# Kernel optimization log

Hardware: AMD Instinct MI355X
Metric: run time of the kernel (lower is better)

The kernel has to match this reference:

```python
import jax, jax.numpy as jnp
import numpy as np

N = 100000          # nodes
E = 3200000         # edges (avg degree 32)
F_IN = 128
HID = [128, 256, 128, 64, 32]
EPS = 1e-5


def setup_inputs() -> dict:
    key = jax.random.key(0)
    ks = jax.random.split(key, 64)
    inp = {}
    inp["x"] = jax.random.normal(ks[0], (N, F_IN), dtype=jnp.float32)
    inp["edge_index"] = jax.random.randint(ks[1], (2, E), 0, N, dtype=jnp.int64)
    dims = [F_IN] + HID
    k = 2
    for i in range(len(HID)):
        fan_in = dims[i]
        inp[f"W{i}"] = jax.random.normal(ks[k], (dims[i], dims[i + 1]), dtype=jnp.float32) / np.sqrt(fan_in); k += 1
        inp[f"b{i}"] = jnp.zeros((dims[i + 1],), dtype=jnp.float32)
        inp[f"g{i}"] = jnp.ones((dims[i + 1],), dtype=jnp.float32)
        inp[f"be{i}"] = jnp.zeros((dims[i + 1],), dtype=jnp.float32)
    inp["fc_w"] = jax.random.normal(ks[k], (HID[-1], 1), dtype=jnp.float32) / np.sqrt(HID[-1])
    inp["fc_b"] = jnp.zeros((1,), dtype=jnp.float32)
    return inp


def _gcn_forward(x, edge_index, Ws, bs, gs, bes, fc_w, fc_b):
    src, dst = edge_index[0], edge_index[1]
    # symmetric-normalized adjacency with self-loops (PyG GCNConv default,
    # edge_weight=None -> all-ones). deg = in-degree + 1 (self-loop).
    deg = jax.ops.segment_sum(jnp.ones((E,), x.dtype), dst, num_segments=N) + 1.0
    dis = jax.lax.rsqrt(deg)                 # deg^{-1/2}
    di = 1.0 / deg                           # self-loop norm deg^{-1}
    norm = (dis[src] * dis[dst])[:, None]    # [E,1]
    for W, b, g, be in zip(Ws, bs, gs, bes):
        h = x @ W                                                        # [N,d']
        x = jax.ops.segment_sum(norm * h[src], dst, num_segments=N)
        x = x + di[:, None] * h + b                                      # conv out
        mu = jnp.mean(x, axis=0)
        var = jnp.mean(jnp.square(x - mu), axis=0)
        x = (x - mu) * jax.lax.rsqrt(var + EPS) * g + be                 # BatchNorm1d
        x = jax.nn.relu(x)                                               # dropout = eval identity
    edge_emb = x[src] * x[dst]                                           # [E, 32]
    return jax.nn.sigmoid(edge_emb @ fc_w + fc_b)                        # [E, 1]


def reference(x, edge_index, W0, b0, g0, be0, W1, b1, g1, be1, W2, b2, g2, be2,
              W3, b3, g3, be3, W4, b4, g4, be4, fc_w, fc_b):
    Ws = [W0, W1, W2, W3, W4]
    bs = [b0, b1, b2, b3, b4]
    gs = [g0, g1, g2, g3, g4]
    bes = [be0, be1, be2, be3, be4]
    return _gcn_forward(x, edge_index, Ws, bs, gs, bes, fc_w, fc_b)
```

## Files before the change

kernel.cpp:

```cpp
#include <hip/hip_runtime.h>
#include <hip/hip_fp16.h>
#include <cstddef>

#define NN 100000
#define EE 3200000
#define EPSB 1e-5f
#define NB 391
#define BCAP 10240
#define BNBLK 512

typedef _Float16 half8 __attribute__((ext_vector_type(8)));
typedef float floatx4 __attribute__((ext_vector_type(4)));


__global__ __launch_bounds__(256) void k_bscat(const int* __restrict__ src,
                                               const int* __restrict__ dst,
                                               int* __restrict__ bcur,
                                               unsigned* __restrict__ barr) {
    __shared__ int hist[NB];
    __shared__ int base[NB];
    int tid = threadIdx.x;
    for (int b = tid; b < NB; b += 256) hist[b] = 0;
    __syncthreads();
    int e0 = blockIdx.x * 4096;
    int d[16], s[16];
    #pragma unroll
    for (int j = 0; j < 16; j++) {
        int e = e0 + j * 256 + tid;
        if (e < EE) {
            d[j] = dst[e];
            s[j] = src[e];
            atomicAdd(&hist[d[j] >> 8], 1);
        } else d[j] = -1;
    }
    __syncthreads();
    for (int b = tid; b < NB; b += 256) {
        int c = hist[b];
        base[b] = (c > 0) ? atomicAdd(&bcur[b], c) : 0;
        hist[b] = 0;
    }
    __syncthreads();
    #pragma unroll
    for (int j = 0; j < 16; j++) {
        if (d[j] >= 0) {
            int b = d[j] >> 8;
            int r = atomicAdd(&hist[b], 1);
            barr[(size_t)b * BCAP + base[b] + r] =
                (unsigned)s[j] | ((unsigned)(d[j] & 255) << 17);
        }
    }
}

__global__ __launch_bounds__(1024) void k_bdeg(const int* __restrict__ bcur,
                                               const unsigned* __restrict__ barr,
                                               int* __restrict__ degcnt,
                                               float* __restrict__ dis) {
    __shared__ int h[256];
    int b = blockIdx.x;
    if (threadIdx.x < 256) h[threadIdx.x] = 0;
    __syncthreads();
    int cnt = bcur[b];
    const unsigned* p = barr + (size_t)b * BCAP;
    for (int t = threadIdx.x; t < cnt; t += 1024)
        atomicAdd(&h[(p[t] >> 17) & 255], 1);
    __syncthreads();
    if (threadIdx.x < 256) {
        int node = (b << 8) + threadIdx.x;
        if (node < NN) {
            int dg = h[threadIdx.x];
            degcnt[node] = dg;
            dis[node] = rsqrtf((float)dg + 1.0f);
        }
    }
}

__global__ __launch_bounds__(1024) void k_place(const int* __restrict__ bcur,
                                                const unsigned* __restrict__ barr,
                                                const int* __restrict__ rowptr,
                                                int* __restrict__ col) {
    __shared__ int cur[256];
    int b = blockIdx.x;
    if (threadIdx.x < 256) {
        int node = (b << 8) + threadIdx.x;
        cur[threadIdx.x] = (node < NN) ? rowptr[node] : 0;
    }
    __syncthreads();
    int cnt = bcur[b];
    const unsigned* p = barr + (size_t)b * BCAP;
    for (int t = threadIdx.x; t < cnt; t += 1024) {
        unsigned e = p[t];
        int pos = atomicAdd(&cur[(e >> 17) & 255], 1);
        col[pos] = (int)(e & 0x1FFFFu);
    }
}

__global__ void k_scan_block(const int* __restrict__ in, int* __restrict__ out,
                             int* __restrict__ blksum, int n) {
    __shared__ int s[1024];
    int i = blockIdx.x * 1024 + threadIdx.x;
    int v = (i < n) ? in[i] : 0;
    s[threadIdx.x] = v;
    __syncthreads();
    for (int off = 1; off < 1024; off <<= 1) {
        int t = (threadIdx.x >= off) ? s[threadIdx.x - off] : 0;
        __syncthreads();
        s[threadIdx.x] += t;
        __syncthreads();
    }
    if (i < n) out[i] = s[threadIdx.x] - v;
    if (threadIdx.x == 1023) blksum[blockIdx.x] = s[1023];
}

__global__ void k_scan_top(int* __restrict__ blksum, int nb) {
    if (threadIdx.x == 0) {
        int acc = 0;
        for (int b = 0; b < nb; b++) { int v = blksum[b]; blksum[b] = acc; acc += v; }
    }
}

__global__ void k_scan_add(int* __restrict__ out, const int* __restrict__ blksum, int n) {
    int i = blockIdx.x * 1024 + threadIdx.x;
    if (i < n) out[i] += blksum[blockIdx.x];
}


__global__ void k_f2h(const float4* __restrict__ in, uint2* __restrict__ out, int n4) {
    int t = blockIdx.x * blockDim.x + threadIdx.x;
    if (t >= n4) return;
    float4 v = in[t];
    union { __half2 h; unsigned u; } a, b;
    a.h = __floats2half2_rn(v.x, v.y);
    b.h = __floats2half2_rn(v.z, v.w);
    out[t] = make_uint2(a.u, b.u);
}

__global__ void k_wpack_all(const float* __restrict__ W0, const float* __restrict__ W1,
                            const float* __restrict__ W2, const float* __restrict__ W3,
                            const float* __restrict__ W4, __half* __restrict__ Wp) {
    const int offs[6] = {0, 16384, 49152, 81920, 90112, 92160};
    const int Ks[5] = {128, 128, 256, 128, 64};
    const int Ns[5] = {128, 256, 128, 64, 32};
    const float* Ws[5] = {W0, W1, W2, W3, W4};
    int t = blockIdx.x * blockDim.x + threadIdx.x;
    if (t >= 92160) return;
    int l = 0;
    while (t >= offs[l + 1]) l++;
    int local = t - offs[l];
    int N = Ns[l], K = Ks[l];
    int k = local / N, n = local - k * N;
    Wp[(size_t)offs[l] + (size_t)n * K + k] = __float2half(Ws[l][local]);
}


template<int NT, bool OUT16, bool ABN>
__global__ __launch_bounds__(256) void k_mgemm(const void* __restrict__ Av,
                                               const __half* __restrict__ Wp,
                                               void* __restrict__ Cv,
                                               int M, int K, int N,
                                               const float* __restrict__ dis,
                                               const float* __restrict__ bias,
                                               const float* __restrict__ AB) {
    constexpr int TN = NT * 16;
    __shared__ __half Ash[128][40];
    __shared__ __half Bsh[TN][40];
    int tid  = threadIdx.x;
    int wave = tid >> 6;
    int lane = tid & 63;
    int quad = lane >> 4;
    int l16  = lane & 15;
    int bm = blockIdx.x * 128;
    int bn = blockIdx.y * TN;

    floatx4 acc[2][NT];
    #pragma unroll
    for (int mt = 0; mt < 2; mt++)
        #pragma unroll
        for (int nt = 0; nt < NT; nt++)
            acc[mt][nt] = (floatx4){0.f, 0.f, 0.f, 0.f};

    for (int k0 = 0; k0 < K; k0 += 32) {
        #pragma unroll
        for (int it = 0; it < 2; it++) {
            int u = tid + it * 256;
            int row = u >> 2, seg = u & 3;
            int grow = bm + row;
            if (ABN) {
                const float* Af = (const float*)Av;
                int f0 = k0 + seg * 8;
                uint4 o = make_uint4(0, 0, 0, 0);
                if (grow < M) {
                    float4 x0 = *(const float4*)&Af[(size_t)grow * K + f0];
                    float4 x1 = *(const float4*)&Af[(size_t)grow * K + f0 + 4];
                    float4 a0 = *(const float4*)&AB[f0];
                    float4 a1 = *(const float4*)&AB[f0 + 4];
                    float4 c0 = *(const float4*)&AB[K + f0];
                    float4 c1 = *(const float4*)&AB[K + f0 + 4];
                    float h0 = fmaxf(x0.x * a0.x + c0.x, 0.f);
                    float h1 = fmaxf(x0.y * a0.y + c0.y, 0.f);
                    float h2 = fmaxf(x0.z * a0.z + c0.z, 0.f);
                    float h3 = fmaxf(x0.w * a0.w + c0.w, 0.f);
                    float h4 = fmaxf(x1.x * a1.x + c1.x, 0.f);
                    float h5 = fmaxf(x1.y * a1.y + c1.y, 0.f);
                    float h6 = fmaxf(x1.z * a1.z + c1.z, 0.f);
                    float h7 = fmaxf(x1.w * a1.w + c1.w, 0.f);
                    union { __half2 h; unsigned u; } p0, p1, p2, p3;
                    p0.h = __floats2half2_rn(h0, h1);
                    p1.h = __floats2half2_rn(h2, h3);
                    p2.h = __floats2half2_rn(h4, h5);
                    p3.h = __floats2half2_rn(h6, h7);
                    o = make_uint4(p0.u, p1.u, p2.u, p3.u);
                }
                *(uint4*)&Ash[row][seg * 8] = o;
            } else {
                const __half* A = (const __half*)Av;
                uint4 v = make_uint4(0, 0, 0, 0);
                if (grow < M) v = *(const uint4*)&A[(size_t)grow * K + k0 + seg * 8];
                *(uint4*)&Ash[row][seg * 8] = v;
            }
        }
        if (tid < TN * 4) {
            int n = tid >> 2, seg = tid & 3;
            uint4 v = *(const uint4*)&Wp[(size_t)(bn + n) * K + k0 + seg * 8];
            *(uint4*)&Bsh[n][seg * 8] = v;
        }
        __syncthreads();
        half8 a[2], b[NT];
        #pragma unroll
        for (int mt = 0; mt < 2; mt++)
            a[mt] = *(const half8*)&Ash[wave * 32 + mt * 16 + l16][quad * 8];
        #pragma unroll
        for (int nt = 0; nt < NT; nt++)
            b[nt] = *(const half8*)&Bsh[nt * 16 + l16][quad * 8];
        #pragma unroll
        for (int mt = 0; mt < 2; mt++)
            #pragma unroll
            for (int nt = 0; nt < NT; nt++)
                acc[mt][nt] = __builtin_amdgcn_mfma_f32_16x16x32_f16(
                    a[mt], b[nt], acc[mt][nt], 0, 0, 0);
        __syncthreads();
    }

    #pragma unroll
    for (int mt = 0; mt < 2; mt++) {
        #pragma unroll
        for (int r = 0; r < 4; r++) {
            int grow = bm + wave * 32 + mt * 16 + quad * 4 + r;
            if (grow >= M) continue;
            if (OUT16) {
                float ds = dis[grow];
                __half* C = (__half*)Cv;
                #pragma unroll
                for (int nt = 0; nt < NT; nt++) {
                    int gcol = bn + nt * 16 + l16;
                    C[(size_t)grow * N + gcol] = __float2half(ds * acc[mt][nt][r]);
                }
            } else {
                float* C = (float*)Cv;
                #pragma unroll
                for (int nt = 0; nt < NT; nt++) {
                    int gcol = bn + nt * 16 + l16;
                    C[(size_t)grow * N + gcol] = acc[mt][nt][r] + bias[gcol];
                }
            }
        }
    }
}


__global__ __launch_bounds__(256) void k_q8p8(const uint4* __restrict__ H,
                                              uint2* __restrict__ q8,
                                              float* __restrict__ scq, int total) {
    int t = blockIdx.x * 256 + threadIdx.x;
    if (t >= total) return;
    uint4 v = H[t];
    const __half2* hp = (const __half2*)&v;
    float h[8];
    #pragma unroll
    for (int k = 0; k < 4; k++) {
        float2 f = __half22float2(hp[k]);
        h[2 * k] = f.x; h[2 * k + 1] = f.y;
    }
    float m = fabsf(h[0]);
    #pragma unroll
    for (int k = 1; k < 8; k++) m = fmaxf(m, fabsf(h[k]));
    float inv = m > 0.f ? 127.f / m : 0.f;
    unsigned b[8];
    #pragma unroll
    for (int k = 0; k < 8; k++) {
        float f = fminf(fmaxf(h[k] * inv, -127.f), 127.f);
        b[k] = (unsigned)(f + 128.5f);
    }
    q8[t] = make_uint2(b[0] | (b[1] << 8) | (b[2] << 16) | (b[3] << 24),
                       b[4] | (b[5] << 8) | (b[6] << 16) | (b[7] << 24));
    scq[t] = m * (1.f / 127.f);
}

__global__ void k_nscale_q8(const float* __restrict__ X, const float* __restrict__ AB,
                            const float* __restrict__ dis, uint2* __restrict__ q8,
                            float* __restrict__ scq) {
    int t = blockIdx.x * blockDim.x + threadIdx.x;
    if (t >= NN * 16) return;
    int row = t >> 4;
    int f0 = (t & 15) * 8;
    float ds = dis[row];
    float4 x0 = *(const float4*)&X[(size_t)row * 128 + f0];
    float4 x1 = *(const float4*)&X[(size_t)row * 128 + f0 + 4];
    float4 a0 = *(const float4*)&AB[f0];
    float4 a1 = *(const float4*)&AB[f0 + 4];
    float4 c0 = *(const float4*)&AB[128 + f0];
    float4 c1 = *(const float4*)&AB[128 + f0 + 4];
    float h[8];
    h[0] = ds * fmaxf(x0.x * a0.x + c0.x, 0.f);
    h[1] = ds * fmaxf(x0.y * a0.y + c0.y, 0.f);
    h[2] = ds * fmaxf(x0.z * a0.z + c0.z, 0.f);
    h[3] = ds * fmaxf(x0.w * a0.w + c0.w, 0.f);
    h[4] = ds * fmaxf(x1.x * a1.x + c1.x, 0.f);
    h[5] = ds * fmaxf(x1.y * a1.y + c1.y, 0.f);
    h[6] = ds * fmaxf(x1.z * a1.z + c1.z, 0.f);
    h[7] = ds * fmaxf(x1.w * a1.w + c1.w, 0.f);
    float m = h[0];
    #pragma unroll
    for (int k = 1; k < 8; k++) m = fmaxf(m, h[k]);
    m = fmaxf(m, __shfl_xor(m, 1));
    float inv = m > 0.f ? 255.f / m : 0.f;
    unsigned b[8];
    #pragma unroll
    for (int k = 0; k < 8; k++)
        b[k] = (unsigned)(fminf(h[k] * inv, 255.f) + 0.5f);
    q8[t] = make_uint2(b[0] | (b[1] << 8) | (b[2] << 16) | (b[3] << 24),
                       b[4] | (b[5] << 8) | (b[6] << 16) | (b[7] << 24));
    if ((t & 1) == 0) scq[t >> 1] = m * (1.f / 255.f);
}


__device__ __forceinline__ void acc_q8s2(float* acc, const uint4& r,
                                         const float2& s, float& c0, float& c1) {
    const unsigned* w = (const unsigned*)&r;
    c0 += s.x; c1 += s.y;
    #pragma unroll
    for (int q = 0; q < 4; q++) {
        unsigned v = w[q];
        float sq = (q < 2) ? s.x : s.y;
        acc[4 * q + 0] = fmaf(sq, (float)(v & 0xffu), acc[4 * q + 0]);
        acc[4 * q + 1] = fmaf(sq, (float)((v >> 8) & 0xffu), acc[4 * q + 1]);
        acc[4 * q + 2] = fmaf(sq, (float)((v >> 16) & 0xffu), acc[4 * q + 2]);
        acc[4 * q + 3] = fmaf(sq, (float)(v >> 24), acc[4 * q + 3]);
    }
}

template<int TPN>
__global__ __launch_bounds__(256) void k_agg_q8s(const uint4* __restrict__ Q,
                                                 const float* __restrict__ sc,
                                                 float* __restrict__ outf,
                                                 const int* __restrict__ rowptr,
                                                 const int* __restrict__ degcnt,
                                                 const int* __restrict__ colv,
                                                 const float* __restrict__ dis,
                                                 const float* __restrict__ bias) {
    constexpr int G = 256 / TPN;
    int g    = threadIdx.x / TPN;
    int lane = threadIdx.x % TPN;
    int i = blockIdx.x * G + g;
    if (i >= NN) return;
    int beg = rowptr[i];
    int cnt = degcnt[i];
    const uint4*  base = Q + lane;
    const float2* scb  = (const float2*)sc + lane;
    float acc[16] = {};
    float c0 = 0.f, c1 = 0.f;
    int e = 0;
    for (; e + 8 <= cnt; e += 8) {
        int c[8];
        #pragma unroll
        for (int j = 0; j < 8; j++) c[j] = colv[beg + e + j];
        uint4 r[8];
        float2 s[8];
        #pragma unroll
        for (int j = 0; j < 8; j++) {
            r[j] = base[(size_t)c[j] * TPN];
            s[j] = scb[(size_t)c[j] * TPN];
        }
        #pragma unroll
        for (int j = 0; j < 8; j++) acc_q8s2(acc, r[j], s[j], c0, c1);
    }
    for (; e < cnt; e++) {
        int c = colv[beg + e];
        uint4 r = base[(size_t)c * TPN];
        acc_q8s2(acc, r, scb[(size_t)c * TPN], c0, c1);
    }
    uint4 rs = base[(size_t)i * TPN];
    acc_q8s2(acc, rs, scb[(size_t)i * TPN], c0, c1);
    float ds = dis[i];
    float zp0 = 128.f * c0, zp1 = 128.f * c1;
    float o[16];
    #pragma unroll
    for (int k = 0; k < 16; k++) o[k] = ds * (acc[k] - (k < 8 ? zp0 : zp1));
    float4* out = (float4*)outf;
    const float4* bi = (const float4*)bias;
    size_t ob = (size_t)i * (4 * TPN) + lane * 4;
    #pragma unroll
    for (int j = 0; j < 4; j++) {
        float4 b = bi[lane * 4 + j];
        out[ob + j] = make_float4(o[4 * j] + b.x, o[4 * j + 1] + b.y,
                                  o[4 * j + 2] + b.z, o[4 * j + 3] + b.w);
    }
}

__device__ __forceinline__ void acc_q8u(float* acc, const uint4& r, float s) {
    const unsigned* w = (const unsigned*)&r;
    #pragma unroll
    for (int q = 0; q < 4; q++) {
        unsigned v = w[q];
        acc[4 * q + 0] = fmaf(s, (float)(v & 0xffu), acc[4 * q + 0]);
        acc[4 * q + 1] = fmaf(s, (float)((v >> 8) & 0xffu), acc[4 * q + 1]);
        acc[4 * q + 2] = fmaf(s, (float)((v >> 16) & 0xffu), acc[4 * q + 2]);
        acc[4 * q + 3] = fmaf(s, (float)(v >> 24), acc[4 * q + 3]);
    }
}

template<int TPN>
__global__ __launch_bounds__(256) void k_agg_q8u(const uint4* __restrict__ Q,
                                                 const float* __restrict__ sc,
                                                 __half* __restrict__ out16,
                                                 const int* __restrict__ rowptr,
                                                 const int* __restrict__ degcnt,
                                                 const int* __restrict__ colv,
                                                 const float* __restrict__ dis) {
    constexpr int G = 256 / TPN;
    int g    = threadIdx.x / TPN;
    int lane = threadIdx.x % TPN;
    int i = blockIdx.x * G + g;
    if (i >= NN) return;
    int beg = rowptr[i];
    int cnt = degcnt[i];
    const uint4* base = Q + lane;
    const float* scb  = sc + lane;
    float acc[16] = {};
    int e = 0;
    for (; e + 8 <= cnt; e += 8) {
        int c[8];
        #pragma unroll
        for (int j = 0; j < 8; j++) c[j] = colv[beg + e + j];
        uint4 r[8];
        float s[8];
        #pragma unroll
        for (int j = 0; j < 8; j++) {
            r[j] = base[(size_t)c[j] * TPN];
            s[j] = scb[(size_t)c[j] * TPN];
        }
        #pragma unroll
        for (int j = 0; j < 8; j++) acc_q8u(acc, r[j], s[j]);
    }
    for (; e < cnt; e++) {
        int c = colv[beg + e];
        uint4 r = base[(size_t)c * TPN];
        acc_q8u(acc, r, scb[(size_t)c * TPN]);
    }
    uint4 rs = base[(size_t)i * TPN];
    acc_q8u(acc, rs, scb[(size_t)i * TPN]);
    float ds = dis[i];
    float o[16];
    #pragma unroll
    for (int k = 0; k < 16; k++) o[k] = ds * acc[k];
    uint4 ov0, ov1;
    __half2* p0 = (__half2*)&ov0;
    __half2* p1 = (__half2*)&ov1;
    #pragma unroll
    for (int k = 0; k < 4; k++) {
        p0[k] = __floats2half2_rn(o[2 * k], o[2 * k + 1]);
        p1[k] = __floats2half2_rn(o[8 + 2 * k], o[9 + 2 * k]);
    }
    uint4* out = (uint4*)out16;
    size_t ob = (size_t)i * (2 * TPN) + lane * 2;
    out[ob]     = ov0;
    out[ob + 1] = ov1;
}

__device__ __forceinline__ void acc_row(float* acc, const uint4& r) {
    const __half2* hp = (const __half2*)&r;
    #pragma unroll
    for (int k = 0; k < 4; k++) {
        float2 f2 = __half22float2(hp[k]);
        acc[2 * k]     += f2.x;
        acc[2 * k + 1] += f2.y;
    }
}

template<int TPN, bool OUT16>
__global__ __launch_bounds__(256) void k_agg_h(const uint4* __restrict__ Hs,
                                               void* __restrict__ outv,
                                               const int* __restrict__ rowptr,
                                               const int* __restrict__ degcnt,
                                               const int* __restrict__ colv,
                                               const float* __restrict__ dis,
                                               const float* __restrict__ bias) {
    constexpr int G = 256 / TPN;
    int g    = threadIdx.x / TPN;
    int lane = threadIdx.x % TPN;
    int i = blockIdx.x * G + g;
    if (i >= NN) return;
    int beg = rowptr[i];
    int cnt = degcnt[i];
    const uint4* base = Hs + lane;
    float acc[8] = {};
    int e = 0;
    for (; e + 16 <= cnt; e += 16) {
        int c[16];
        #pragma unroll
        for (int j = 0; j < 16; j++) c[j] = colv[beg + e + j];
        uint4 r[16];
        #pragma unroll
        for (int j = 0; j < 16; j++) r[j] = base[(size_t)c[j] * TPN];
        #pragma unroll
        for (int j = 0; j < 16; j++) acc_row(acc, r[j]);
    }
    for (; e + 4 <= cnt; e += 4) {
        int c[4];
        #pragma unroll
        for (int j = 0; j < 4; j++) c[j] = colv[beg + e + j];
        uint4 r[4];
        #pragma unroll
        for (int j = 0; j < 4; j++) r[j] = base[(size_t)c[j] * TPN];
        #pragma unroll
        for (int j = 0; j < 4; j++) acc_row(acc, r[j]);
    }
    for (; e < cnt; e++) {
        uint4 r = base[(size_t)colv[beg + e] * TPN];
        acc_row(acc, r);
    }
    uint4 rs = base[(size_t)i * TPN];
    acc_row(acc, rs);
    float ds = dis[i];
    float o[8];
    #pragma unroll
    for (int k = 0; k < 8; k++) o[k] = ds * acc[k];
    if (OUT16) {
        uint4 ov;
        __half2* op = (__half2*)&ov;
        #pragma unroll
        for (int k = 0; k < 4; k++) op[k] = __floats2half2_rn(o[2 * k], o[2 * k + 1]);
        ((uint4*)outv)[(size_t)i * TPN + lane] = ov;
    } else {
        float4 b0 = ((const float4*)bias)[lane * 2];
        float4 b1 = ((const float4*)bias)[lane * 2 + 1];
        o[0] += b0.x; o[1] += b0.y; o[2] += b0.z; o[3] += b0.w;
        o[4] += b1.x; o[5] += b1.y; o[6] += b1.z; o[7] += b1.w;
        float4* out = (float4*)outv;
        size_t ob = (size_t)i * (2 * TPN) + lane * 2;
        out[ob]     = make_float4(o[0], o[1], o[2], o[3]);
        out[ob + 1] = make_float4(o[4], o[5], o[6], o[7]);
    }
}


template<int D>
__global__ __launch_bounds__(256) void k_bnpart(const float4* __restrict__ X4,
                                                float* __restrict__ partial) {
    constexpr int Q   = D / 4;
    constexpr int RPI = 256 / Q;
    int tq = threadIdx.x % Q;
    int rg = threadIdx.x / Q;
    int chunk = (NN + BNBLK - 1) / BNBLK;
    int r0 = blockIdx.x * chunk;
    int r1 = r0 + chunk; if (r1 > NN) r1 = NN;
    float4 s  = {0.f, 0.f, 0.f, 0.f};
    float4 s2 = {0.f, 0.f, 0.f, 0.f};
    for (int r = r0 + rg; r < r1; r += RPI) {
        float4 v = X4[(size_t)r * Q + tq];
        s.x += v.x; s.y += v.y; s.z += v.z; s.w += v.w;
        s2.x += v.x * v.x; s2.y += v.y * v.y; s2.z += v.z * v.z; s2.w += v.w * v.w;
    }
    __shared__ float4 ls[256], ls2[256];
    ls[threadIdx.x] = s; ls2[threadIdx.x] = s2;
    __syncthreads();
    if (threadIdx.x < Q) {
        float4 a = ls[threadIdx.x], b = ls2[threadIdx.x];
        #pragma unroll
        for (int g = 1; g < RPI; g++) {
            float4 u = ls[g * Q + threadIdx.x], w = ls2[g * Q + threadIdx.x];
            a.x += u.x; a.y += u.y; a.z += u.z; a.w += u.w;
            b.x += w.x; b.y += w.y; b.z += w.z; b.w += w.w;
        }
        *(float4*)&partial[(size_t)blockIdx.x * 2 * D + threadIdx.x * 4]     = a;
        *(float4*)&partial[(size_t)blockIdx.x * 2 * D + D + threadIdx.x * 4] = b;
    }
}

template<int D>
__global__ __launch_bounds__(1024) void k_bnfin2(const float* __restrict__ partial,
                                                 const float* __restrict__ g,
                                                 const float* __restrict__ be,
                                                 float* __restrict__ AB) {
    constexpr int G = 1024 / D;
    int f  = threadIdx.x % D;
    int gr = threadIdx.x / D;
    float sum = 0.f, sq = 0.f;
    for (int b = gr; b < BNBLK; b += G) {
        sum += partial[(size_t)b * 2 * D + f];
        sq  += partial[(size_t)b * 2 * D + D + f];
    }
    __shared__ float ls[1024], ls2[1024];
    ls[threadIdx.x] = sum; ls2[threadIdx.x] = sq;
    __syncthreads();
    if (threadIdx.x < D) {
        float a = ls[threadIdx.x], b = ls2[threadIdx.x];
        for (int k = 1; k < G; k++) {
            a += ls[k * D + threadIdx.x];
            b += ls2[k * D + threadIdx.x];
        }
        float mu  = a / (float)NN;
        float var = b / (float)NN - mu * mu;
        var = fmaxf(var, 0.f);
        float inv = rsqrtf(var + EPSB);
        float sc = g[threadIdx.x] * inv;
        AB[threadIdx.x]     = sc;
        AB[D + threadIdx.x] = be[threadIdx.x] - mu * sc;
    }
}

__global__ void k_norm16(const float4* __restrict__ X, const float* __restrict__ AB,
                         uint2* __restrict__ Y, int d, int total4) {
    int t = blockIdx.x * blockDim.x + threadIdx.x;
    if (t >= total4) return;
    int f0 = (t * 4) & (d - 1);
    float4 v = X[t];
    float a0 = AB[f0],     a1 = AB[f0 + 1], a2 = AB[f0 + 2], a3 = AB[f0 + 3];
    float c0 = AB[d + f0], c1 = AB[d + f0 + 1], c2 = AB[d + f0 + 2], c3 = AB[d + f0 + 3];
    float o0 = fmaxf(v.x * a0 + c0, 0.f);
    float o1 = fmaxf(v.y * a1 + c1, 0.f);
    float o2 = fmaxf(v.z * a2 + c2, 0.f);
    float o3 = fmaxf(v.w * a3 + c3, 0.f);
    union { __half2 h; unsigned u; } p, q;
    p.h = __floats2half2_rn(o0, o1);
    q.h = __floats2half2_rn(o2, o3);
    Y[t] = make_uint2(p.u, q.u);
}


__global__ __launch_bounds__(256) void k_edge16(const uint4* __restrict__ X,
                                                const int* __restrict__ src,
                                                const int* __restrict__ dst,
                                                const float* __restrict__ fcw,
                                                const float* __restrict__ fcb,
                                                float* __restrict__ out) {
    int lane = threadIdx.x & 3;
    size_t t = (size_t)blockIdx.x * 256 + threadIdx.x;
    int eid = (int)(t >> 2);
    if (eid >= EE) return;
    int s = src[eid], d = dst[eid];
    uint4 av = X[(size_t)s * 4 + lane];
    uint4 bv = X[(size_t)d * 4 + lane];
    const __half2* ap = (const __half2*)&av;
    const __half2* bp2 = (const __half2*)&bv;
    float v = 0.f;
    #pragma unroll
    for (int k = 0; k < 4; k++) {
        float2 fa = __half22float2(ap[k]);
        float2 fb = __half22float2(bp2[k]);
        float w0 = fcw[lane * 8 + 2 * k];
        float w1 = fcw[lane * 8 + 2 * k + 1];
        v += fa.x * fb.x * w0 + fa.y * fb.y * w1;
    }
    v += __shfl_xor(v, 1, 4);
    v += __shfl_xor(v, 2, 4);
    if (lane == 0) out[eid] = 1.f / (1.f + expf(-(v + fcb[0])));
}


extern "C" void kernel_launch(void* const* d_in, const int* in_sizes, int n_in,
                              void* d_out, int out_size, void* d_ws, size_t ws_size,
                              hipStream_t stream) {
    const float* x0 = (const float*)d_in[0];
    const int* ei   = (const int*)d_in[1];
    const int* srcv = ei;
    const int* dstv = ei + EE;
    const float *W[5], *bp[5], *gp[5], *bep[5];
    int idx = 2;
    for (int l = 0; l < 5; l++) {
        W[l]   = (const float*)d_in[idx++];
        bp[l]  = (const float*)d_in[idx++];
        gp[l]  = (const float*)d_in[idx++];
        bep[l] = (const float*)d_in[idx++];
    }
    const float* fcw = (const float*)d_in[22];
    const float* fcb = (const float*)d_in[23];

    char* ws = (char*)d_ws;
    size_t off = 0;
    auto alloc = [&](size_t bytes) -> void* {
        void* p = ws + off;
        off = (off + bytes + 255) & ~(size_t)255;
        return p;
    };
    float*    bufA    = (float*)   alloc((size_t)NN * 256 * 4);
    __half*   act16   = (__half*)  alloc((size_t)NN * 256 * 2);
    __half*   x16     = (__half*)  alloc((size_t)NN * 128 * 2);
    __half*   Hh      = (__half*)  alloc((size_t)NN * 128 * 2);
    unsigned* barr    = (unsigned*)alloc((size_t)NB * BCAP * 4);
    int*      colv    = (int*)     alloc((size_t)EE * 4);
    int*      rowptr  = (int*)     alloc((size_t)NN * 4);
    int*      degcnt  = (int*)     alloc((size_t)NN * 4);
    float*    dis     = (float*)   alloc((size_t)NN * 4);
    int*      bcur    = (int*)     alloc((size_t)NB * 4);
    int*      scnblk  = (int*)     alloc(4096);
    float*    bnpart  = (float*)   alloc((size_t)BNBLK * 512 * 4);
    float*    bnAB    = (float*)   alloc(512 * 4);
    __half*   Wp      = (__half*)  alloc((size_t)92160 * 2);
    float*    scq     = (float*)   alloc((size_t)NN * 16 * 4);
    const int woff[5] = {0, 16384, 49152, 81920, 90112};

    unsigned char* q8 = (unsigned char*)barr;

    hipMemsetAsync(bcur, 0, (size_t)NB * 4, stream);
    k_bscat<<<(EE + 4095) / 4096, 256, 0, stream>>>(srcv, dstv, bcur, barr);
    k_bdeg<<<NB, 1024, 0, stream>>>(bcur, barr, degcnt, dis);
    int nScanBlk = (NN + 1023) / 1024;
    k_scan_block<<<nScanBlk, 1024, 0, stream>>>(degcnt, rowptr, scnblk, NN);
    k_scan_top<<<1, 64, 0, stream>>>(scnblk, nScanBlk);
    k_scan_add<<<nScanBlk, 1024, 0, stream>>>(rowptr, scnblk, NN);
    k_place<<<NB, 1024, 0, stream>>>(bcur, barr, rowptr, colv);

    k_f2h<<<(NN * 128 / 4 + 255) / 256, 256, 0, stream>>>(
        (const float4*)x0, (uint2*)x16, NN * 128 / 4);
    k_wpack_all<<<(92160 + 255) / 256, 256, 0, stream>>>(W[0], W[1], W[2], W[3], W[4], Wp);

    int gx = (NN + 127) / 128;

    {
        dim3 grid(gx, 128 / 64);
        k_mgemm<4, true, false><<<grid, 256, 0, stream>>>(x16, Wp + woff[0], Hh, NN, 128, 128, dis, nullptr, nullptr);
        k_q8p8<<<NN * 16 / 256, 256, 0, stream>>>((const uint4*)Hh, (uint2*)q8, scq, NN * 16);
        k_agg_q8s<8><<<(NN + 31) / 32, 256, 0, stream>>>(
            (const uint4*)q8, scq, bufA, rowptr, degcnt, colv, dis, bp[0]);
        k_bnpart<128><<<BNBLK, 256, 0, stream>>>((const float4*)bufA, bnpart);
        k_bnfin2<128><<<1, 1024, 0, stream>>>(bnpart, gp[0], bep[0], bnAB);
        k_nscale_q8<<<(NN * 16 + 255) / 256, 256, 0, stream>>>(bufA, bnAB, dis, (uint2*)q8, scq);
    }
    {
        k_agg_q8u<8><<<(NN + 31) / 32, 256, 0, stream>>>(
            (const uint4*)q8, scq, act16, rowptr, degcnt, colv, dis);
        dim3 grid(gx, 256 / 64);
        k_mgemm<4, false, false><<<grid, 256, 0, stream>>>(act16, Wp + woff[1], bufA, NN, 128, 256, nullptr, bp[1], nullptr);
        k_bnpart<256><<<BNBLK, 256, 0, stream>>>((const float4*)bufA, bnpart);
        k_bnfin2<256><<<1, 1024, 0, stream>>>(bnpart, gp[1], bep[1], bnAB);
    }
    {
        dim3 grid(gx, 128 / 64);
        k_mgemm<4, true, true><<<grid, 256, 0, stream>>>(bufA, Wp + woff[2], Hh, NN, 256, 128, dis, nullptr, bnAB);
        k_agg_h<16, false><<<(NN + 15) / 16, 256, 0, stream>>>(
            (const uint4*)Hh, bufA, rowptr, degcnt, colv, dis, bp[2]);
        k_bnpart<128><<<BNBLK, 256, 0, stream>>>((const float4*)bufA, bnpart);
        k_bnfin2<128><<<1, 1024, 0, stream>>>(bnpart, gp[2], bep[2], bnAB);
    }
    {
        dim3 grid(gx, 64 / 64);
        k_mgemm<4, true, true><<<grid, 256, 0, stream>>>(bufA, Wp + woff[3], Hh, NN, 128, 64, dis, nullptr, bnAB);
        k_agg_h<8, false><<<(NN + 31) / 32, 256, 0, stream>>>(
            (const uint4*)Hh, bufA, rowptr, degcnt, colv, dis, bp[3]);
        k_bnpart<64><<<BNBLK, 256, 0, stream>>>((const float4*)bufA, bnpart);
        k_bnfin2<64><<<1, 1024, 0, stream>>>(bnpart, gp[3], bep[3], bnAB);
    }
    {
        dim3 grid(gx, 1);
        k_mgemm<2, true, true><<<grid, 256, 0, stream>>>(bufA, Wp + woff[4], Hh, NN, 64, 32, dis, nullptr, bnAB);
        k_agg_h<4, false><<<(NN + 63) / 64, 256, 0, stream>>>(
            (const uint4*)Hh, bufA, rowptr, degcnt, colv, dis, bp[4]);
        k_bnpart<32><<<BNBLK, 256, 0, stream>>>((const float4*)bufA, bnpart);
        k_bnfin2<32><<<1, 1024, 0, stream>>>(bnpart, gp[4], bep[4], bnAB);
        int total4 = NN * 32 / 4;
        k_norm16<<<(total4 + 255) / 256, 256, 0, stream>>>(
            (const float4*)bufA, bnAB, (uint2*)act16, 32, total4);
    }

    size_t edgeThreads = (size_t)EE * 4;
    k_edge16<<<(unsigned)((edgeThreads + 255) / 256), 256, 0, stream>>>(
        (const uint4*)act16, srcv, dstv, fcw, fcb, (float*)d_out);
}
```

Before: 984.5 us.

## Store conv outputs in fp16 and fuse BatchNorm partial sums into aggregation

Conv-layer outputs are now stored as fp16 instead of fp32. The aggregation kernels also compute per-block sum and sum-of-squares partials through shared memory. This removes most separate BatchNorm-partial passes and halves the intermediate read/write traffic. In exchange the finalize kernel reads many more partials (one per aggregation block), and storing pre-BN activations in fp16 adds precision risk.

```diff
diff --git a/kernel.cpp b/kernel.cpp
--- a/kernel.cpp
+++ b/kernel.cpp
@@ -152,7 +152,7 @@
 }
 
 
-template<int NT, bool OUT16, bool ABN>
+template<int NT, bool OUT16, bool ABN, bool AH16, bool CH16>
 __global__ __launch_bounds__(256) void k_mgemm(const void* __restrict__ Av,
                                                const __half* __restrict__ Wp,
                                                void* __restrict__ Cv,
@@ -185,24 +185,38 @@
             int row = u >> 2, seg = u & 3;
             int grow = bm + row;
             if (ABN) {
-                const float* Af = (const float*)Av;
                 int f0 = k0 + seg * 8;
                 uint4 o = make_uint4(0, 0, 0, 0);
                 if (grow < M) {
-                    float4 x0 = *(const float4*)&Af[(size_t)grow * K + f0];
-                    float4 x1 = *(const float4*)&Af[(size_t)grow * K + f0 + 4];
+                    float x[8];
+                    if (AH16) {
+                        const __half* Af = (const __half*)Av;
+                        uint4 xv = *(const uint4*)&Af[(size_t)grow * K + f0];
+                        const __half2* xp = (const __half2*)&xv;
+                        #pragma unroll
+                        for (int k = 0; k < 4; k++) {
+                            float2 f = __half22float2(xp[k]);
+                            x[2 * k] = f.x; x[2 * k + 1] = f.y;
+                        }
+                    } else {
+                        const float* Af = (const float*)Av;
+                        float4 x0 = *(const float4*)&Af[(size_t)grow * K + f0];
+                        float4 x1 = *(const float4*)&Af[(size_t)grow * K + f0 + 4];
+                        x[0] = x0.x; x[1] = x0.y; x[2] = x0.z; x[3] = x0.w;
+                        x[4] = x1.x; x[5] = x1.y; x[6] = x1.z; x[7] = x1.w;
+                    }
                     float4 a0 = *(const float4*)&AB[f0];
                     float4 a1 = *(const float4*)&AB[f0 + 4];
                     float4 c0 = *(const float4*)&AB[K + f0];
                     float4 c1 = *(const float4*)&AB[K + f0 + 4];
-                    float h0 = fmaxf(x0.x * a0.x + c0.x, 0.f);
-                    float h1 = fmaxf(x0.y * a0.y + c0.y, 0.f);
-                    float h2 = fmaxf(x0.z * a0.z + c0.z, 0.f);
-                    float h3 = fmaxf(x0.w * a0.w + c0.w, 0.f);
-                    float h4 = fmaxf(x1.x * a1.x + c1.x, 0.f);
-                    float h5 = fmaxf(x1.y * a1.y + c1.y, 0.f);
-                    float h6 = fmaxf(x1.z * a1.z + c1.z, 0.f);
-                    float h7 = fmaxf(x1.w * a1.w + c1.w, 0.f);
+                    float h0 = fmaxf(x[0] * a0.x + c0.x, 0.f);
+                    float h1 = fmaxf(x[1] * a0.y + c0.y, 0.f);
+                    float h2 = fmaxf(x[2] * a0.z + c0.z, 0.f);
+                    float h3 = fmaxf(x[3] * a0.w + c0.w, 0.f);
+                    float h4 = fmaxf(x[4] * a1.x + c1.x, 0.f);
+                    float h5 = fmaxf(x[5] * a1.y + c1.y, 0.f);
+                    float h6 = fmaxf(x[6] * a1.z + c1.z, 0.f);
+                    float h7 = fmaxf(x[7] * a1.w + c1.w, 0.f);
                     union { __half2 h; unsigned u; } p0, p1, p2, p3;
                     p0.h = __floats2half2_rn(h0, h1);
                     p1.h = __floats2half2_rn(h2, h3);
@@ -254,6 +268,13 @@
                     int gcol = bn + nt * 16 + l16;
                     C[(size_t)grow * N + gcol] = __float2half(ds * acc[mt][nt][r]);
                 }
+            } else if (CH16) {
+                __half* C = (__half*)Cv;
+                #pragma unroll
+                for (int nt = 0; nt < NT; nt++) {
+                    int gcol = bn + nt * 16 + l16;
+                    C[(size_t)grow * N + gcol] = __float2half(acc[mt][nt][r] + bias[gcol]);
+                }
             } else {
                 float* C = (float*)Cv;
                 #pragma unroll
@@ -295,29 +316,36 @@
     scq[t] = m * (1.f / 127.f);
 }
 
-__global__ void k_nscale_q8(const float* __restrict__ X, const float* __restrict__ AB,
+__global__ void k_nscale_q8(const __half* __restrict__ X, const float* __restrict__ AB,
                             const float* __restrict__ dis, uint2* __restrict__ q8,
                             float* __restrict__ scq) {
     int t = blockIdx.x * blockDim.x + threadIdx.x;
     if (t >= NN * 16) return;
     int row = t >> 4;
-    int f0 = (t & 15) * 8;
+    int sub = t & 15;
+    int f0 = sub * 8;
     float ds = dis[row];
-    float4 x0 = *(const float4*)&X[(size_t)row * 128 + f0];
-    float4 x1 = *(const float4*)&X[(size_t)row * 128 + f0 + 4];
+    uint4 xv = ((const uint4*)X)[(size_t)row * 16 + sub];
+    const __half2* xp = (const __half2*)&xv;
+    float x[8];
+    #pragma unroll
+    for (int k = 0; k < 4; k++) {
+        float2 f = __half22float2(xp[k]);
+        x[2 * k] = f.x; x[2 * k + 1] = f.y;
+    }
     float4 a0 = *(const float4*)&AB[f0];
     float4 a1 = *(const float4*)&AB[f0 + 4];
     float4 c0 = *(const float4*)&AB[128 + f0];
     float4 c1 = *(const float4*)&AB[128 + f0 + 4];
     float h[8];
-    h[0] = ds * fmaxf(x0.x * a0.x + c0.x, 0.f);
-    h[1] = ds * fmaxf(x0.y * a0.y + c0.y, 0.f);
-    h[2] = ds * fmaxf(x0.z * a0.z + c0.z, 0.f);
-    h[3] = ds * fmaxf(x0.w * a0.w + c0.w, 0.f);
-    h[4] = ds * fmaxf(x1.x * a1.x + c1.x, 0.f);
-    h[5] = ds * fmaxf(x1.y * a1.y + c1.y, 0.f);
-    h[6] = ds * fmaxf(x1.z * a1.z + c1.z, 0.f);
-    h[7] = ds * fmaxf(x1.w * a1.w + c1.w, 0.f);
+    h[0] = ds * fmaxf(x[0] * a0.x + c0.x, 0.f);
+    h[1] = ds * fmaxf(x[1] * a0.y + c0.y, 0.f);
+    h[2] = ds * fmaxf(x[2] * a0.z + c0.z, 0.f);
+    h[3] = ds * fmaxf(x[3] * a0.w + c0.w, 0.f);
+    h[4] = ds * fmaxf(x[4] * a1.x + c1.x, 0.f);
+    h[5] = ds * fmaxf(x[5] * a1.y + c1.y, 0.f);
+    h[6] = ds * fmaxf(x[6] * a1.z + c1.z, 0.f);
+    h[7] = ds * fmaxf(x[7] * a1.w + c1.w, 0.f);
     float m = h[0];
     #pragma unroll
     for (int k = 1; k < 8; k++) m = fmaxf(m, h[k]);
@@ -348,22 +376,21 @@
     }
 }
 
-template<int TPN>
 __global__ __launch_bounds__(256) void k_agg_q8s(const uint4* __restrict__ Q,
                                                  const float* __restrict__ sc,
-                                                 float* __restrict__ outf,
+                                                 __half* __restrict__ outh,
                                                  const int* __restrict__ rowptr,
                                                  const int* __restrict__ degcnt,
                                                  const int* __restrict__ colv,
                                                  const float* __restrict__ dis,
-                                                 const float* __restrict__ bias) {
-    constexpr int G = 256 / TPN;
-    int g    = threadIdx.x / TPN;
-    int lane = threadIdx.x % TPN;
-    int i = blockIdx.x * G + g;
-    if (i >= NN) return;
-    int beg = rowptr[i];
-    int cnt = degcnt[i];
+                                                 const float* __restrict__ bias,
+                                                 float* __restrict__ part) {
+    int g    = threadIdx.x >> 3;
+    int lane = threadIdx.x & 7;
+    int i = blockIdx.x * 32 + g;
+    bool alive = i < NN;
+    int beg = alive ? rowptr[i] : 0;
+    int cnt = alive ? degcnt[i] : 0;
     const uint4*  base = Q + lane;
     const float2* scb  = (const float2*)sc + lane;
     float acc[16] = {};
@@ -377,32 +404,55 @@
         float2 s[8];
         #pragma unroll
         for (int j = 0; j < 8; j++) {
-            r[j] = base[(size_t)c[j] * TPN];
-            s[j] = scb[(size_t)c[j] * TPN];
+            r[j] = base[(size_t)c[j] * 8];
+            s[j] = scb[(size_t)c[j] * 8];
         }
         #pragma unroll
         for (int j = 0; j < 8; j++) acc_q8s2(acc, r[j], s[j], c0, c1);
     }
     for (; e < cnt; e++) {
         int c = colv[beg + e];
-        uint4 r = base[(size_t)c * TPN];
-        acc_q8s2(acc, r, scb[(size_t)c * TPN], c0, c1);
-    }
-    uint4 rs = base[(size_t)i * TPN];
-    acc_q8s2(acc, rs, scb[(size_t)i * TPN], c0, c1);
-    float ds = dis[i];
+        acc_q8s2(acc, base[(size_t)c * 8], scb[(size_t)c * 8], c0, c1);
+    }
+    if (alive) acc_q8s2(acc, base[(size_t)i * 8], scb[(size_t)i * 8], c0, c1);
+    float ds = alive ? dis[i] : 0.f;
     float zp0 = 128.f * c0, zp1 = 128.f * c1;
+    const float4* bi = (const float4*)bias;
     float o[16];
-    #pragma unroll
-    for (int k = 0; k < 16; k++) o[k] = ds * (acc[k] - (k < 8 ? zp0 : zp1));
-    float4* out = (float4*)outf;
-    const float4* bi = (const float4*)bias;
-    size_t ob = (size_t)i * (4 * TPN) + lane * 4;
     #pragma unroll
     for (int j = 0; j < 4; j++) {
         float4 b = bi[lane * 4 + j];
-        out[ob + j] = make_float4(o[4 * j] + b.x, o[4 * j + 1] + b.y,
-                                  o[4 * j + 2] + b.z, o[4 * j + 3] + b.w);
+        o[4 * j + 0] = alive ? ds * (acc[4 * j + 0] - (j < 2 ? zp0 : zp1)) + b.x : 0.f;
+        o[4 * j + 1] = alive ? ds * (acc[4 * j + 1] - (j < 2 ? zp0 : zp1)) + b.y : 0.f;
+        o[4 * j + 2] = alive ? ds * (acc[4 * j + 2] - (j < 2 ? zp0 : zp1)) + b.z : 0.f;
+        o[4 * j + 3] = alive ? ds * (acc[4 * j + 3] - (j < 2 ? zp0 : zp1)) + b.w : 0.f;
+    }
+    if (alive) {
+        uint4 ov0, ov1;
+        __half2* p0 = (__half2*)&ov0;
+        __half2* p1 = (__half2*)&ov1;
+        #pragma unroll
+        for (int k = 0; k < 4; k++) {
+            p0[k] = __floats2half2_rn(o[2 * k], o[2 * k + 1]);
+            p1[k] = __floats2half2_rn(o[8 + 2 * k], o[9 + 2 * k]);
+        }
+        uint4* out = (uint4*)outh;
+        out[(size_t)i * 16 + lane * 2]     = ov0;
+        out[(size_t)i * 16 + lane * 2 + 1] = ov1;
+    }
+    __shared__ float lsh[32][129];
+    #pragma unroll
+    for (int k = 0; k < 16; k++) lsh[g][lane * 16 + k] = o[k];
+    __syncthreads();
+    if (threadIdx.x < 128) {
+        float s = 0.f, q = 0.f;
+        #pragma unroll 4
+        for (int gg = 0; gg < 32; gg++) {
+            float v = lsh[gg][threadIdx.x];
+            s += v; q += v * v;
+        }
+        part[(size_t)blockIdx.x * 256 + threadIdx.x]       = s;
+        part[(size_t)blockIdx.x * 256 + 128 + threadIdx.x] = q;
     }
 }
 
@@ -418,7 +468,6 @@
     }
 }
 
-template<int TPN>
 __global__ __launch_bounds__(256) void k_agg_q8u(const uint4* __restrict__ Q,
                                                  const float* __restrict__ sc,
                                                  __half* __restrict__ out16,
@@ -426,10 +475,9 @@
                                                  const int* __restrict__ degcnt,
                                                  const int* __restrict__ colv,
                                                  const float* __restrict__ dis) {
-    constexpr int G = 256 / TPN;
-    int g    = threadIdx.x / TPN;
-    int lane = threadIdx.x % TPN;
-    int i = blockIdx.x * G + g;
+    int g    = threadIdx.x >> 3;
+    int lane = threadIdx.x & 7;
+    int i = blockIdx.x * 32 + g;
     if (i >= NN) return;
     int beg = rowptr[i];
     int cnt = degcnt[i];
@@ -445,19 +493,17 @@
         float s[8];
         #pragma unroll
         for (int j = 0; j < 8; j++) {
-            r[j] = base[(size_t)c[j] * TPN];
-            s[j] = scb[(size_t)c[j] * TPN];
+            r[j] = base[(size_t)c[j] * 8];
+            s[j] = scb[(size_t)c[j] * 8];
         }
         #pragma unroll
         for (int j = 0; j < 8; j++) acc_q8u(acc, r[j], s[j]);
     }
     for (; e < cnt; e++) {
         int c = colv[beg + e];
-        uint4 r = base[(size_t)c * TPN];
-        acc_q8u(acc, r, scb[(size_t)c * TPN]);
-    }
-    uint4 rs = base[(size_t)i * TPN];
-    acc_q8u(acc, rs, scb[(size_t)i * TPN]);
+        acc_q8u(acc, base[(size_t)c * 8], scb[(size_t)c * 8]);
+    }
+    acc_q8u(acc, base[(size_t)i * 8], scb[(size_t)i * 8]);
     float ds = dis[i];
     float o[16];
     #pragma unroll
@@ -471,9 +517,8 @@
         p1[k] = __floats2half2_rn(o[8 + 2 * k], o[9 + 2 * k]);
     }
     uint4* out = (uint4*)out16;
-    size_t ob = (size_t)i * (2 * TPN) + lane * 2;
-    out[ob]     = ov0;
-    out[ob + 1] = ov1;
+    out[(size_t)i * 16 + lane * 2]     = ov0;
+    out[(size_t)i * 16 + lane * 2 + 1] = ov1;
 }
 
 __device__ __forceinline__ void acc_row(float* acc, const uint4& r) {
@@ -486,108 +531,127 @@
     }
 }
 
-template<int TPN, bool OUT16>
-__global__ __launch_bounds__(256) void k_agg_h(const uint4* __restrict__ Hs,
-                                               void* __restrict__ outv,
-                                               const int* __restrict__ rowptr,
-                                               const int* __restrict__ degcnt,
-                                               const int* __restrict__ colv,
-                                               const float* __restrict__ dis,
-                                               const float* __restrict__ bias) {
+template<int TPN>
+__global__ __launch_bounds__(256) void k_agg_hf(const uint4* __restrict__ Hs,
+                                                __half* __restrict__ outh,
+                                                const int* __restrict__ rowptr,
+                                                const int* __restrict__ degcnt,
+                                                const int* __restrict__ colv,
+                                                const float* __restrict__ dis,
+                                                const float* __restrict__ bias,
+                                                float* __restrict__ part) {
     constexpr int G = 256 / TPN;
+    constexpr int D = TPN * 8;
     int g    = threadIdx.x / TPN;
     int lane = threadIdx.x % TPN;
     int i = blockIdx.x * G + g;
-    if (i >= NN) return;
-    int beg = rowptr[i];
-    int cnt = degcnt[i];
+    bool alive = i < NN;
+    int beg = alive ? rowptr[i] : 0;
+    int cnt = alive ? degcnt[i] : 0;
     const uint4* base = Hs + lane;
     float acc[8] = {};
     int e = 0;
-    for (; e + 16 <= cnt; e += 16) {
-        int c[16];
-        #pragma unroll
-        for (int j = 0; j < 16; j++) c[j] = colv[beg + e + j];
-        uint4 r[16];
-        #pragma unroll
-        for (int j = 0; j < 16; j++) r[j] = base[(size_t)c[j] * TPN];
-        #pragma unroll
-        for (int j = 0; j < 16; j++) acc_row(acc, r[j]);
-    }
-    for (; e + 4 <= cnt; e += 4) {
-        int c[4];
-        #pragma unroll
-        for (int j = 0; j < 4; j++) c[j] = colv[beg + e + j];
-        uint4 r[4];
-        #pragma unroll
-        for (int j = 0; j < 4; j++) r[j] = base[(size_t)c[j] * TPN];
-        #pragma unroll
-        for (int j = 0; j < 4; j++) acc_row(acc, r[j]);
+    for (; e + 8 <= cnt; e += 8) {
+        int c[8];
+        #pragma unroll
+        for (int j = 0; j < 8; j++) c[j] = colv[beg + e + j];
+        uint4 r[8];
+        #pragma unroll
+        for (int j = 0; j < 8; j++) r[j] = base[(size_t)c[j] * TPN];
+        #pragma unroll
+        for (int j = 0; j < 8; j++) acc_row(acc, r[j]);
     }
     for (; e < cnt; e++) {
         uint4 r = base[(size_t)colv[beg + e] * TPN];
         acc_row(acc, r);
     }
-    uint4 rs = base[(size_t)i * TPN];
-    acc_row(acc, rs);
-    float ds = dis[i];
+    if (alive) {
+        uint4 rs = base[(size_t)i * TPN];
+        acc_row(acc, rs);
+    }
+    float ds = alive ? dis[i] : 0.f;
+    float4 b0 = ((const float4*)bias)[lane * 2];
+    float4 b1 = ((const float4*)bias)[lane * 2 + 1];
     float o[8];
-    #pragma unroll
-    for (int k = 0; k < 8; k++) o[k] = ds * acc[k];
-    if (OUT16) {
+    o[0] = alive ? ds * acc[0] + b0.x : 0.f;
+    o[1] = alive ? ds * acc[1] + b0.y : 0.f;
+    o[2] = alive ? ds * acc[2] + b0.z : 0.f;
+    o[3] = alive ? ds * acc[3] + b0.w : 0.f;
+    o[4] = alive ? ds * acc[4] + b1.x : 0.f;
+    o[5] = alive ? ds * acc[5] + b1.y : 0.f;
+    o[6] = alive ? ds * acc[6] + b1.z : 0.f;
+    o[7] = alive ? ds * acc[7] + b1.w : 0.f;
+    if (alive) {
         uint4 ov;
         __half2* op = (__half2*)&ov;
         #pragma unroll
         for (int k = 0; k < 4; k++) op[k] = __floats2half2_rn(o[2 * k], o[2 * k + 1]);
-        ((uint4*)outv)[(size_t)i * TPN + lane] = ov;
-    } else {
-        float4 b0 = ((const float4*)bias)[lane * 2];
-        float4 b1 = ((const float4*)bias)[lane * 2 + 1];
-        o[0] += b0.x; o[1] += b0.y; o[2] += b0.z; o[3] += b0.w;
-        o[4] += b1.x; o[5] += b1.y; o[6] += b1.z; o[7] += b1.w;
-        float4* out = (float4*)outv;
-        size_t ob = (size_t)i * (2 * TPN) + lane * 2;
-        out[ob]     = make_float4(o[0], o[1], o[2], o[3]);
-        out[ob + 1] = make_float4(o[4], o[5], o[6], o[7]);
+        ((uint4*)outh)[(size_t)i * TPN + lane] = ov;
+    }
+    __shared__ float lsh[G][D + 1];
+    #pragma unroll
+    for (int k = 0; k < 8; k++) lsh[g][lane * 8 + k] = o[k];
+    __syncthreads();
+    if (threadIdx.x < D) {
+        float s = 0.f, q = 0.f;
+        #pragma unroll 4
+        for (int gg = 0; gg < G; gg++) {
+            float v = lsh[gg][threadIdx.x];
+            s += v; q += v * v;
+        }
+        part[(size_t)blockIdx.x * (2 * D) + threadIdx.x]     = s;
+        part[(size_t)blockIdx.x * (2 * D) + D + threadIdx.x] = q;
     }
 }
 
 
 template<int D>
-__global__ __launch_bounds__(256) void k_bnpart(const float4* __restrict__ X4,
-                                                float* __restrict__ partial) {
-    constexpr int Q   = D / 4;
+__global__ __launch_bounds__(256) void k_bnpart_h(const uint4* __restrict__ X,
+                                                  float* __restrict__ partial) {
+    constexpr int Q   = D / 8;
     constexpr int RPI = 256 / Q;
     int tq = threadIdx.x % Q;
     int rg = threadIdx.x / Q;
     int chunk = (NN + BNBLK - 1) / BNBLK;
     int r0 = blockIdx.x * chunk;
     int r1 = r0 + chunk; if (r1 > NN) r1 = NN;
-    float4 s  = {0.f, 0.f, 0.f, 0.f};
-    float4 s2 = {0.f, 0.f, 0.f, 0.f};
+    float s[8] = {}, q2[8] = {};
     for (int r = r0 + rg; r < r1; r += RPI) {
-        float4 v = X4[(size_t)r * Q + tq];
-        s.x += v.x; s.y += v.y; s.z += v.z; s.w += v.w;
-        s2.x += v.x * v.x; s2.y += v.y * v.y; s2.z += v.z * v.z; s2.w += v.w * v.w;
-    }
-    __shared__ float4 ls[256], ls2[256];
-    ls[threadIdx.x] = s; ls2[threadIdx.x] = s2;
+        uint4 v = X[(size_t)r * Q + tq];
+        const __half2* hp = (const __half2*)&v;
+        #pragma unroll
+        for (int k = 0; k < 4; k++) {
+            float2 f = __half22float2(hp[k]);
+            s[2 * k] += f.x;  s[2 * k + 1] += f.y;
+            q2[2 * k] += f.x * f.x; q2[2 * k + 1] += f.y * f.y;
+        }
+    }
+    __shared__ float ls[2048], ls2[2048];
+    #pragma unroll
+    for (int k = 0; k < 8; k++) {
+        ls[threadIdx.x * 8 + k]  = s[k];
+        ls2[threadIdx.x * 8 + k] = q2[k];
+    }
     __syncthreads();
     if (threadIdx.x < Q) {
-        float4 a = ls[threadIdx.x], b = ls2[threadIdx.x];
-        #pragma unroll
-        for (int g = 1; g < RPI; g++) {
-            float4 u = ls[g * Q + threadIdx.x], w = ls2[g * Q + threadIdx.x];
-            a.x += u.x; a.y += u.y; a.z += u.z; a.w += u.w;
-            b.x += w.x; b.y += w.y; b.z += w.z; b.w += w.w;
-        }
-        *(float4*)&partial[(size_t)blockIdx.x * 2 * D + threadIdx.x * 4]     = a;
-        *(float4*)&partial[(size_t)blockIdx.x * 2 * D + D + threadIdx.x * 4] = b;
+        #pragma unroll 2
+        for (int g = 1; g < RPI; g++)
+            #pragma unroll
+            for (int k = 0; k < 8; k++) {
+                s[k]  += ls[(g * Q + threadIdx.x) * 8 + k];
+                q2[k] += ls2[(g * Q + threadIdx.x) * 8 + k];
+            }
+        #pragma unroll
+        for (int k = 0; k < 8; k++) {
+            partial[(size_t)blockIdx.x * 2 * D + threadIdx.x * 8 + k]     = s[k];
+            partial[(size_t)blockIdx.x * 2 * D + D + threadIdx.x * 8 + k] = q2[k];
+        }
     }
 }
 
 template<int D>
-__global__ __launch_bounds__(1024) void k_bnfin2(const float* __restrict__ partial,
+__global__ __launch_bounds__(1024) void k_bnfinP(const float* __restrict__ partial,
+                                                 int P,
                                                  const float* __restrict__ g,
                                                  const float* __restrict__ be,
                                                  float* __restrict__ AB) {
@@ -595,7 +659,7 @@
     int f  = threadIdx.x % D;
     int gr = threadIdx.x / D;
     float sum = 0.f, sq = 0.f;
-    for (int b = gr; b < BNBLK; b += G) {
+    for (int b = gr; b < P; b += G) {
         sum += partial[(size_t)b * 2 * D + f];
         sq  += partial[(size_t)b * 2 * D + D + f];
     }
@@ -618,22 +682,28 @@
     }
 }
 
-__global__ void k_norm16(const float4* __restrict__ X, const float* __restrict__ AB,
-                         uint2* __restrict__ Y, int d, int total4) {
+__global__ void k_norm16h(const uint4* __restrict__ X, const float* __restrict__ AB,
+                          uint4* __restrict__ Y) {
     int t = blockIdx.x * blockDim.x + threadIdx.x;
-    if (t >= total4) return;
-    int f0 = (t * 4) & (d - 1);
-    float4 v = X[t];
-    float a0 = AB[f0],     a1 = AB[f0 + 1], a2 = AB[f0 + 2], a3 = AB[f0 + 3];
-    float c0 = AB[d + f0], c1 = AB[d + f0 + 1], c2 = AB[d + f0 + 2], c3 = AB[d + f0 + 3];
-    float o0 = fmaxf(v.x * a0 + c0, 0.f);
-    float o1 = fmaxf(v.y * a1 + c1, 0.f);
-    float o2 = fmaxf(v.z * a2 + c2, 0.f);
-    float o3 = fmaxf(v.w * a3 + c3, 0.f);
-    union { __half2 h; unsigned u; } p, q;
-    p.h = __floats2half2_rn(o0, o1);
-    q.h = __floats2half2_rn(o2, o3);
-    Y[t] = make_uint2(p.u, q.u);
+    if (t >= NN * 4) return;
+    int f0 = (t & 3) * 8;
+    uint4 v = X[t];
+    const __half2* hp = (const __half2*)&v;
+    float x[8];
+    #pragma unroll
+    for (int k = 0; k < 4; k++) {
+        float2 f = __half22float2(hp[k]);
+        x[2 * k] = f.x; x[2 * k + 1] = f.y;
+    }
+    uint4 ov;
+    __half2* op = (__half2*)&ov;
+    #pragma unroll
+    for (int k = 0; k < 4; k++) {
+        float o0 = fmaxf(x[2 * k] * AB[f0 + 2 * k] + AB[32 + f0 + 2 * k], 0.f);
+        float o1 = fmaxf(x[2 * k + 1] * AB[f0 + 2 * k + 1] + AB[32 + f0 + 2 * k + 1], 0.f);
+        op[k] = __floats2half2_rn(o0, o1);
+    }
+    Y[t] = ov;
 }
 
 
@@ -692,7 +762,7 @@
         off = (off + bytes + 255) & ~(size_t)255;
         return p;
     };
-    float*    bufA    = (float*)   alloc((size_t)NN * 256 * 4);
+    __half*   conv16  = (__half*)  alloc((size_t)NN * 256 * 2);
     __half*   act16   = (__half*)  alloc((size_t)NN * 256 * 2);
     __half*   x16     = (__half*)  alloc((size_t)NN * 128 * 2);
     __half*   Hh      = (__half*)  alloc((size_t)NN * 128 * 2);
@@ -703,7 +773,7 @@
     float*    dis     = (float*)   alloc((size_t)NN * 4);
     int*      bcur    = (int*)     alloc((size_t)NB * 4);
     int*      scnblk  = (int*)     alloc(4096);
-    float*    bnpart  = (float*)   alloc((size_t)BNBLK * 512 * 4);
+    float*    part    = (float*)   alloc((size_t)6250 * 256 * 4);
     float*    bnAB    = (float*)   alloc(512 * 4);
     __half*   Wp      = (__half*)  alloc((size_t)92160 * 2);
     float*    scq     = (float*)   alloc((size_t)NN * 16 * 4);
@@ -728,48 +798,48 @@
 
     {
         dim3 grid(gx, 128 / 64);
-        k_mgemm<4, true, false><<<grid, 256, 0, stream>>>(x16, Wp + woff[0], Hh, NN, 128, 128, dis, nullptr, nullptr);
+        k_mgemm<4, true, false, false, false><<<grid, 256, 0, stream>>>(
+            x16, Wp + woff[0], Hh, NN, 128, 128, dis, nullptr, nullptr);
         k_q8p8<<<NN * 16 / 256, 256, 0, stream>>>((const uint4*)Hh, (uint2*)q8, scq, NN * 16);
-        k_agg_q8s<8><<<(NN + 31) / 32, 256, 0, stream>>>(
-            (const uint4*)q8, scq, bufA, rowptr, degcnt, colv, dis, bp[0]);
-        k_bnpart<128><<<BNBLK, 256, 0, stream>>>((const float4*)bufA, bnpart);
-        k_bnfin2<128><<<1, 1024, 0, stream>>>(bnpart, gp[0], bep[0], bnAB);
-        k_nscale_q8<<<(NN * 16 + 255) / 256, 256, 0, stream>>>(bufA, bnAB, dis, (uint2*)q8, scq);
+        k_agg_q8s<<<(NN + 31) / 32, 256, 0, stream>>>(
+            (const uint4*)q8, scq, conv16, rowptr, degcnt, colv, dis, bp[0], part);
+        k_bnfinP<128><<<1, 1024, 0, stream>>>(part, (NN + 31) / 32, gp[0], bep[0], bnAB);
+        k_nscale_q8<<<(NN * 16 + 255) / 256, 256, 0, stream>>>(conv16, bnAB, dis, (uint2*)q8, scq);
     }
     {
-        k_agg_q8u<8><<<(NN + 31) / 32, 256, 0, stream>>>(
+        k_agg_q8u<<<(NN + 31) / 32, 256, 0, stream>>>(
             (const uint4*)q8, scq, act16, rowptr, degcnt, colv, dis);
         dim3 grid(gx, 256 / 64);
-        k_mgemm<4, false, false><<<grid, 256, 0, stream>>>(act16, Wp + woff[1], bufA, NN, 128, 256, nullptr, bp[1], nullptr);
-        k_bnpart<256><<<BNBLK, 256, 0, stream>>>((const float4*)bufA, bnpart);
-        k_bnfin2<256><<<1, 1024, 0, stream>>>(bnpart, gp[1], bep[1], bnAB);
+        k_mgemm<4, false, false, false, true><<<grid, 256, 0, stream>>>(
+            act16, Wp + woff[1], conv16, NN, 128, 256, nullptr, bp[1], nullptr);
+        k_bnpart_h<256><<<BNBLK, 256, 0, stream>>>((const uint4*)conv16, part);
+        k_bnfinP<256><<<1, 1024, 0, stream>>>(part, BNBLK, gp[1], bep[1], bnAB);
     }
     {
         dim3 grid(gx, 128 / 64);
-        k_mgemm<4, true, true><<<grid, 256, 0, stream>>>(bufA, Wp + woff[2], Hh, NN, 256, 128, dis, nullptr, bnAB);
-        k_agg_h<16, false><<<(NN + 15) / 16, 256, 0, stream>>>(
-            (const uint4*)Hh, bufA, rowptr, degcnt, colv, dis, bp[2]);
-        k_bnpart<128><<<BNBLK, 256, 0, stream>>>((const float4*)bufA, bnpart);
-        k_bnfin2<128><<<1, 1024, 0, stream>>>(bnpart, gp[2], bep[2], bnAB);
+        k_mgemm<4, true, true, true, false><<<grid, 256, 0, stream>>>(
+            conv16, Wp + woff[2], Hh, NN, 256, 128, dis, nullptr, bnAB);
+        k_agg_hf<16><<<(NN + 15) / 16, 256, 0, stream>>>(
+            (const uint4*)Hh, conv16, rowptr, degcnt, colv, dis, bp[2], part);
+        k_bnfinP<128><<<1, 1024, 0, stream>>>(part, (NN + 15) / 16, gp[2], bep[2], bnAB);
     }
     {
         dim3 grid(gx, 64 / 64);
-        k_mgemm<4, true, true><<<grid, 256, 0, stream>>>(bufA, Wp + woff[3], Hh, NN, 128, 64, dis, nullptr, bnAB);
-        k_agg_h<8, false><<<(NN + 31) / 32, 256, 0, stream>>>(
-            (const uint4*)Hh, bufA, rowptr, degcnt, colv, dis, bp[3]);
-        k_bnpart<64><<<BNBLK, 256, 0, stream>>>((const float4*)bufA, bnpart);
-        k_bnfin2<64><<<1, 1024, 0, stream>>>(bnpart, gp[3], bep[3], bnAB);
+        k_mgemm<4, true, true, true, false><<<grid, 256, 0, stream>>>(
+            conv16, Wp + woff[3], Hh, NN, 128, 64, dis, nullptr, bnAB);
+        k_agg_hf<8><<<(NN + 31) / 32, 256, 0, stream>>>(
+            (const uint4*)Hh, conv16, rowptr, degcnt, colv, dis, bp[3], part);
+        k_bnfinP<64><<<1, 1024, 0, stream>>>(part, (NN + 31) / 32, gp[3], bep[3], bnAB);
     }
     {
         dim3 grid(gx, 1);
-        k_mgemm<2, true, true><<<grid, 256, 0, stream>>>(bufA, Wp + woff[4], Hh, NN, 64, 32, dis, nullptr, bnAB);
-        k_agg_h<4, false><<<(NN + 63) / 64, 256, 0, stream>>>(
-            (const uint4*)Hh, bufA, rowptr, degcnt, colv, dis, bp[4]);
-        k_bnpart<32><<<BNBLK, 256, 0, stream>>>((const float4*)bufA, bnpart);
-        k_bnfin2<32><<<1, 1024, 0, stream>>>(bnpart, gp[4], bep[4], bnAB);
-        int total4 = NN * 32 / 4;
-        k_norm16<<<(total4 + 255) / 256, 256, 0, stream>>>(
-            (const float4*)bufA, bnAB, (uint2*)act16, 32, total4);
+        k_mgemm<2, true, true, true, false><<<grid, 256, 0, stream>>>(
+            conv16, Wp + woff[4], Hh, NN, 64, 32, dis, nullptr, bnAB);
+        k_agg_hf<4><<<(NN + 63) / 64, 256, 0, stream>>>(
+            (const uint4*)Hh, conv16, rowptr, degcnt, colv, dis, bp[4], part);
+        k_bnfinP<32><<<1, 1024, 0, stream>>>(part, (NN + 63) / 64, gp[4], bep[4], bnAB);
+        k_norm16h<<<(NN * 4 + 255) / 256, 256, 0, stream>>>(
+            (const uint4*)conv16, bnAB, (uint4*)act16);
     }
 
     size_t edgeThreads = (size_t)EE * 4;
```

Result: slower. 1.248 ms (+26.8%).
